# Optimization experiments

Measured on AMD Instinct MI355X. Metric: run time of the kernel, lower is better.

## Reference

```python
import jax, jax.numpy as jnp
import numpy as np

N_NODES = 10000
N_EDGES = 640000
D_IN = 128
D_OUT = 128


def setup_inputs() -> dict:
    key = jax.random.key(0)
    k1, k2, k3, k4 = jax.random.split(key, 4)
    x = jax.random.normal(k1, (N_NODES, D_IN), dtype=jnp.float32)
    # PyG GCNConv weight: [dim_out, dim_in] (glorot)
    W = jax.random.normal(k2, (D_OUT, D_IN), dtype=jnp.float32) * (1.0 / np.sqrt(D_IN))
    b = jnp.zeros((D_OUT,), dtype=jnp.float32)
    edge_weight = jax.random.uniform(k3, (N_EDGES,), dtype=jnp.float32)
    edge_index = jax.random.randint(k4, (2, N_EDGES), 0, N_NODES, dtype=jnp.int32)
    return {"x": x, "W": W, "b": b, "edge_weight": edge_weight, "edge_index": edge_index}


def reference(x, W, b, edge_weight, edge_index):
    N = x.shape[0]
    # --- add self loops (fill weight = 1.0), PyG default ---
    loops = jnp.arange(N, dtype=edge_index.dtype)
    src = jnp.concatenate([edge_index[0], loops])
    dst = jnp.concatenate([edge_index[1], loops])
    ew = jnp.concatenate([edge_weight, jnp.ones((N,), dtype=edge_weight.dtype)])
    # --- symmetric GCN normalization: deg from target index ---
    deg = jax.ops.segment_sum(ew, dst, num_segments=N)
    dinv = jnp.where(deg > 0, jax.lax.rsqrt(deg), 0.0)
    norm = dinv[src] * ew * dinv[dst]  # [E+N]
    # --- linear transform then gather-scale-scatter aggregation ---
    h = x @ W.T  # [N, D_OUT]
    msgs = h[src] * norm[:, None]  # [E+N, D_OUT]
    out = jax.ops.segment_sum(msgs, dst, num_segments=N)
    return out + b
```

## Files before the change

kernel.cpp:

```cpp
#include <hip/hip_runtime.h>

#define N_NODES 10000
#define N_EDGES 640000
#define D 128
#define CAP 128

typedef unsigned long long ull;
typedef unsigned short u16;
typedef unsigned int u32;
typedef unsigned char u8;

#define CHUNKS 128
#define EPC 5000
#define GEMM_NPB 32
#define GEMM_BLOCKS ((N_NODES + GEMM_NPB - 1) / GEMM_NPB)
#define SMEM_A 40960
#define EWFX 262144.0f
#define EWM  0x1ffffffu

__device__ __forceinline__ u16 f2bf(float f) {
    unsigned u = __float_as_uint(f);
    unsigned r = (u + 0x7fffu + ((u >> 16) & 1u)) >> 16;
    return (u16)r;
}


__global__ void __launch_bounds__(256) k_build(
    const int* __restrict__ dst, const float* __restrict__ ew,
    const float* __restrict__ x, const float* __restrict__ W,
    u16* __restrict__ h_bf, u32* __restrict__ counts, u8* __restrict__ ranks)
{
    extern __shared__ char smem[];
    const int t = threadIdx.x;

    if (blockIdx.x < CHUNKS) {
        u32* hist = (u32*)smem;
        ull* h8 = (ull*)smem;
        for (int i = t; i < N_NODES / 2; i += 256) h8[i] = 0;
        __syncthreads();

        const int e0 = blockIdx.x * EPC;
        #pragma unroll
        for (int i = 0; i < 20; ++i) {
            int idx = i * 256 + t;
            if (idx < EPC) {
                int e = e0 + idx;
                int d = dst[e];
                u32 add = (1u << 25) | (u32)(ew[e] * EWFX);
                u32 old = atomicAdd(&hist[d], add);
                ranks[e] = (u8)(old >> 25);
            }
        }
        __syncthreads();

        u32* cnt = counts + (size_t)blockIdx.x * N_NODES;
        for (int i = t; i < N_NODES; i += 256) cnt[i] = hist[i];
    } else {
        float* xs = (float*)smem;
        const int node0 = (blockIdx.x - CHUNKS) * GEMM_NPB;
        const int col = t & 127;
        const int half = t >> 7;

        #pragma unroll
        for (int r = 0; r < 16; ++r) {
            int row = half * 16 + r;
            int n = node0 + row;
            xs[row * D + col] = (n < N_NODES) ? x[n * D + col] : 0.0f;
        }
        __syncthreads();

        float acc[16];
        #pragma unroll
        for (int r = 0; r < 16; ++r) acc[r] = 0.0f;

        const float4* Wrow = (const float4*)&W[col * D];
        const float* xbase = &xs[half * 16 * D];
        for (int k4 = 0; k4 < D / 4; ++k4) {
            float4 w = Wrow[k4];
            int k = k4 * 4;
            #pragma unroll
            for (int r = 0; r < 16; ++r) {
                acc[r] += xbase[r * D + k + 0] * w.x;
                acc[r] += xbase[r * D + k + 1] * w.y;
                acc[r] += xbase[r * D + k + 2] * w.z;
                acc[r] += xbase[r * D + k + 3] * w.w;
            }
        }
        #pragma unroll
        for (int r = 0; r < 16; ++r) {
            int n = node0 + half * 16 + r;
            if (n < N_NODES) h_bf[n * D + col] = f2bf(acc[r]);
        }
    }
}


__global__ void __launch_bounds__(256) k_scan(
    u32* __restrict__ counts, u32* __restrict__ gpacked, float* __restrict__ dinv)
{
    const int b = blockIdx.x * 256 + threadIdx.x;
    if (b >= N_NODES) return;
    u32 run = 0;
    #pragma unroll 8
    for (int c = 0; c < CHUNKS; ++c) {
        u32 v = counts[(size_t)c * N_NODES + b];
        counts[(size_t)c * N_NODES + b] = run;
        run += v;
    }
    gpacked[b] = run;
    dinv[b] = rsqrtf(1.0f + (float)(run & EWM) * 0x1p-18f);
}


__global__ void __launch_bounds__(256) k_scatter(
    const int* __restrict__ src, const int* __restrict__ dst,
    const float* __restrict__ ew, const u8* __restrict__ ranks,
    const u32* __restrict__ counts, const float* __restrict__ dinv,
    ull* __restrict__ csr)
{
    __shared__ u16  lbase[N_NODES];
    __shared__ float ldin[N_NODES];
    const int t = threadIdx.x;

    const u32* cnt = counts + (size_t)blockIdx.x * N_NODES;
    for (int i = t; i < N_NODES; i += 256) lbase[i] = (u16)(cnt[i] >> 25);
    for (int i = t; i < N_NODES; i += 256) ldin[i] = dinv[i];
    __syncthreads();

    const int e0 = blockIdx.x * EPC;
    #pragma unroll
    for (int i = 0; i < 20; ++i) {
        int idx = i * 256 + t;
        if (idx < EPC) {
            int e = e0 + idx;
            int d = dst[e];
            int s = src[e];
            float w = ew[e];
            float nm = ldin[d] * w * ldin[s];
            int slot = (int)lbase[d] + (int)ranks[e];
            csr[(size_t)d * CAP + slot] = ((ull)__float_as_uint(nm) << 32) | (u32)s;
        }
    }
}


#define AGG_NPB 4

__global__ void __launch_bounds__(256) k_agg(
    const u32* __restrict__ gpacked, const float* __restrict__ dinv,
    const ull* __restrict__ csr, const u16* __restrict__ h_bf,
    const float* __restrict__ b, float* __restrict__ out)
{
    const int wid  = threadIdx.x >> 6;
    const int lane = threadIdx.x & 63;
    const int n = blockIdx.x * AGG_NPB + wid;

    __shared__ ull sm[AGG_NPB][CAP];

    const int deg = (int)(gpacked[n] >> 25);
    const float dn = dinv[n];
    const ull* bucket = csr + (size_t)n * CAP;

    #pragma unroll
    for (int r = 0; r < 2; ++r) {
        int j = r * 64 + lane;
        if (j < deg) sm[wid][j] = bucket[j];
    }
    __syncthreads();

    float acc0 = 0.0f, acc1 = 0.0f;
    const ull* smw = sm[wid];
    #pragma unroll 4
    for (int j = 0; j < deg; ++j) {
        ull v = smw[j];
        int s = (int)(u32)v;
        float nm = __uint_as_float((u32)(v >> 32));
        u32 hc = *(const u32*)(h_bf + (size_t)s * D + lane * 2);
        acc0 += __uint_as_float(hc << 16) * nm;
        acc1 += __uint_as_float(hc & 0xffff0000u) * nm;
    }

    float s2 = dn * dn;
    u32 hs = *(const u32*)(h_bf + (size_t)n * D + lane * 2);
    acc0 += __uint_as_float(hs << 16) * s2;
    acc1 += __uint_as_float(hs & 0xffff0000u) * s2;
    float2 bb = *(const float2*)(b + lane * 2);
    float2 o;
    o.x = acc0 + bb.x;
    o.y = acc1 + bb.y;
    *(float2*)(out + (size_t)n * D + lane * 2) = o;
}


extern "C" void kernel_launch(void* const* d_in, const int* in_sizes, int n_in,
                              void* d_out, int out_size, void* d_ws, size_t ws_size,
                              hipStream_t stream) {
    const float* x  = (const float*)d_in[0];
    const float* W  = (const float*)d_in[1];
    const float* b  = (const float*)d_in[2];
    const float* ew = (const float*)d_in[3];
    const int* ei   = (const int*)d_in[4];
    const int* src = ei;
    const int* dst = ei + N_EDGES;
    float* out = (float*)d_out;

    char* ws = (char*)d_ws;
    u32*   gpacked = (u32*)(ws);
    float* dinv    = (float*)(ws + 40000);
    u16*   h_bf    = (u16*)(ws + 80000);
    ull*   csr     = (ull*)(ws + 2640000);
    u32*   counts  = (u32*)(ws + 12880000);
    u8*    ranks   = (u8*)(ws + 18000000);

    k_build<<<CHUNKS + GEMM_BLOCKS, 256, SMEM_A, stream>>>(
        dst, ew, x, W, h_bf, counts, ranks);
    k_scan<<<(N_NODES + 255) / 256, 256, 0, stream>>>(counts, gpacked, dinv);
    k_scatter<<<CHUNKS, 256, 0, stream>>>(src, dst, ew, ranks, counts, dinv, csr);
    k_agg<<<N_NODES / AGG_NPB, 256, 0, stream>>>(gpacked, dinv, csr, h_bf, b, out);
}
```

Baseline: 132.1 us.

## Fuse build, scan and scatter into one cooperative kernel with grid syncs

```diff
diff --git a/kernel.cpp b/kernel.cpp
--- a/kernel.cpp
+++ b/kernel.cpp
@@ -1,4 +1,7 @@
 #include <hip/hip_runtime.h>
+#include <hip/hip_cooperative_groups.h>
+
+namespace cg = cooperative_groups;
 
 #define N_NODES 10000
 #define N_EDGES 640000
@@ -8,12 +11,12 @@
 typedef unsigned long long ull;
 typedef unsigned short u16;
 typedef unsigned int u32;
-typedef unsigned char u8;
 
 #define CHUNKS 128
 #define EPC 5000
 #define GEMM_NPB 32
 #define GEMM_BLOCKS ((N_NODES + GEMM_NPB - 1) / GEMM_NPB)
+#define NB (CHUNKS + GEMM_BLOCKS)
 #define SMEM_A 40960
 #define EWFX 262144.0f
 #define EWM  0x1ffffffu
@@ -25,39 +28,49 @@
 }
 
 
-__global__ void __launch_bounds__(256) k_build(
-    const int* __restrict__ dst, const float* __restrict__ ew,
-    const float* __restrict__ x, const float* __restrict__ W,
-    u16* __restrict__ h_bf, u32* __restrict__ counts, u8* __restrict__ ranks)
+__global__ void __launch_bounds__(256, 4) k_coop(
+    const int* __restrict__ src, const int* __restrict__ dst,
+    const float* __restrict__ ew, const float* __restrict__ x,
+    const float* __restrict__ W, u16* __restrict__ h_bf,
+    u32* __restrict__ counts, u32* __restrict__ gpacked,
+    float* __restrict__ dinv, ull* __restrict__ csr)
 {
     extern __shared__ char smem[];
+    cg::grid_group grid = cg::this_grid();
     const int t = threadIdx.x;
-
-    if (blockIdx.x < CHUNKS) {
+    const int bid = blockIdx.x;
+
+    u32  dlr[20];
+    float ewr[20];
+
+    if (bid < CHUNKS) {
         u32* hist = (u32*)smem;
         ull* h8 = (ull*)smem;
         for (int i = t; i < N_NODES / 2; i += 256) h8[i] = 0;
         __syncthreads();
 
-        const int e0 = blockIdx.x * EPC;
+        const int e0 = bid * EPC;
         #pragma unroll
         for (int i = 0; i < 20; ++i) {
             int idx = i * 256 + t;
+            dlr[i] = 0xffffffffu;
             if (idx < EPC) {
                 int e = e0 + idx;
                 int d = dst[e];
-                u32 add = (1u << 25) | (u32)(ew[e] * EWFX);
+                float w = ew[e];
+                ewr[i] = w;
+                u32 add = (1u << 25) | (u32)(w * EWFX);
                 u32 old = atomicAdd(&hist[d], add);
-                ranks[e] = (u8)(old >> 25);
-            }
-        }
-        __syncthreads();
-
-        u32* cnt = counts + (size_t)blockIdx.x * N_NODES;
+                dlr[i] = ((u32)d << 7) | (old >> 25);
+            }
+        }
+        __syncthreads();
+
+        u32* cnt = counts + (size_t)bid * N_NODES;
         for (int i = t; i < N_NODES; i += 256) cnt[i] = hist[i];
     } else {
         float* xs = (float*)smem;
-        const int node0 = (blockIdx.x - CHUNKS) * GEMM_NPB;
+        const int node0 = (bid - CHUNKS) * GEMM_NPB;
         const int col = t & 127;
         const int half = t >> 7;
 
@@ -92,53 +105,43 @@
             if (n < N_NODES) h_bf[n * D + col] = f2bf(acc[r]);
         }
     }
-}
-
-
-__global__ void __launch_bounds__(256) k_scan(
-    u32* __restrict__ counts, u32* __restrict__ gpacked, float* __restrict__ dinv)
-{
-    const int b = blockIdx.x * 256 + threadIdx.x;
-    if (b >= N_NODES) return;
-    u32 run = 0;
-    #pragma unroll 8
-    for (int c = 0; c < CHUNKS; ++c) {
-        u32 v = counts[(size_t)c * N_NODES + b];
-        counts[(size_t)c * N_NODES + b] = run;
-        run += v;
-    }
-    gpacked[b] = run;
-    dinv[b] = rsqrtf(1.0f + (float)(run & EWM) * 0x1p-18f);
-}
-
-
-__global__ void __launch_bounds__(256) k_scatter(
-    const int* __restrict__ src, const int* __restrict__ dst,
-    const float* __restrict__ ew, const u8* __restrict__ ranks,
-    const u32* __restrict__ counts, const float* __restrict__ dinv,
-    ull* __restrict__ csr)
-{
-    __shared__ u16  lbase[N_NODES];
-    __shared__ float ldin[N_NODES];
-    const int t = threadIdx.x;
-
-    const u32* cnt = counts + (size_t)blockIdx.x * N_NODES;
-    for (int i = t; i < N_NODES; i += 256) lbase[i] = (u16)(cnt[i] >> 25);
-    for (int i = t; i < N_NODES; i += 256) ldin[i] = dinv[i];
-    __syncthreads();
-
-    const int e0 = blockIdx.x * EPC;
-    #pragma unroll
-    for (int i = 0; i < 20; ++i) {
-        int idx = i * 256 + t;
-        if (idx < EPC) {
-            int e = e0 + idx;
-            int d = dst[e];
-            int s = src[e];
-            float w = ew[e];
-            float nm = ldin[d] * w * ldin[s];
-            int slot = (int)lbase[d] + (int)ranks[e];
-            csr[(size_t)d * CAP + slot] = ((ull)__float_as_uint(nm) << 32) | (u32)s;
+
+    grid.sync();
+
+    {
+        int b = bid * 256 + t;
+        if (b < N_NODES) {
+            u32 run = 0;
+            #pragma unroll 8
+            for (int c = 0; c < CHUNKS; ++c) {
+                u32 v = counts[(size_t)c * N_NODES + b];
+                counts[(size_t)c * N_NODES + b] = run;
+                run += v;
+            }
+            gpacked[b] = run;
+            dinv[b] = rsqrtf(1.0f + (float)(run & EWM) * 0x1p-18f);
+        }
+    }
+
+    grid.sync();
+
+    if (bid < CHUNKS) {
+        u32* hist = (u32*)smem;
+        const u32* cnt = counts + (size_t)bid * N_NODES;
+        for (int i = t; i < N_NODES; i += 256) hist[i] = cnt[i];
+        __syncthreads();
+
+        const int e0 = bid * EPC;
+        #pragma unroll
+        for (int i = 0; i < 20; ++i) {
+            if (dlr[i] != 0xffffffffu) {
+                int e = e0 + i * 256 + t;
+                int d = (int)(dlr[i] >> 7);
+                int rank = (int)(dlr[i] & 127u);
+                int slot = (int)(hist[d] >> 25) + rank;
+                csr[(size_t)d * CAP + slot] =
+                    ((ull)__float_as_uint(ewr[i]) << 32) | (u32)src[e];
+            }
         }
     }
 }
@@ -164,7 +167,13 @@
     #pragma unroll
     for (int r = 0; r < 2; ++r) {
         int j = r * 64 + lane;
-        if (j < deg) sm[wid][j] = bucket[j];
+        if (j < deg) {
+            ull v = bucket[j];
+            int s = (int)(u32)(v & 0xffffffffu);
+            float w = __uint_as_float((u32)(v >> 32));
+            float nm = dinv[s] * w * dn;
+            sm[wid][j] = ((ull)__float_as_uint(nm) << 32) | (u32)s;
+        }
     }
     __syncthreads();
 
@@ -210,11 +219,12 @@
     u16*   h_bf    = (u16*)(ws + 80000);
     ull*   csr     = (ull*)(ws + 2640000);
     u32*   counts  = (u32*)(ws + 12880000);
-    u8*    ranks   = (u8*)(ws + 18000000);
-
-    k_build<<<CHUNKS + GEMM_BLOCKS, 256, SMEM_A, stream>>>(
-        dst, ew, x, W, h_bf, counts, ranks);
-    k_scan<<<(N_NODES + 255) / 256, 256, 0, stream>>>(counts, gpacked, dinv);
-    k_scatter<<<CHUNKS, 256, 0, stream>>>(src, dst, ew, ranks, counts, dinv, csr);
+
+    void* kargs[] = {
+        (void*)&src, (void*)&dst, (void*)&ew, (void*)&x, (void*)&W,
+        (void*)&h_bf, (void*)&counts, (void*)&gpacked, (void*)&dinv, (void*)&csr
+    };
+    hipLaunchCooperativeKernel((const void*)k_coop, dim3(NB), dim3(256),
+                               kargs, SMEM_A, stream);
     k_agg<<<N_NODES / AGG_NPB, 256, 0, stream>>>(gpacked, dinv, csr, h_bf, b, out);
 }
```

Measured after the change: 236.0 us. 1.79x slower.
